# Kernel optimization log

Hardware: AMD Instinct MI355X
Metric: run time of the kernel (lower is better)

The kernel has to match this reference:

```python
import jax, jax.numpy as jnp
import numpy as np

B, F, D = 1024, 160000, 16


def setup_inputs() -> dict:
    key = jax.random.key(0)
    k1, k2, k3 = jax.random.split(key, 3)
    x = jax.random.randint(k1, (B, F), 0, 2, dtype=jnp.int32)  # multi-hot transaction
    emb_w = jax.random.normal(k2, (F, D), dtype=jnp.float32) * 0.05  # FM factor table
    bias_w = jax.random.normal(k3, (F, 1), dtype=jnp.float32) * 0.05  # per-field linear bias
    g_bias = jnp.zeros((), dtype=jnp.float32)  # global bias
    return {"x": x, "emb_w": emb_w, "bias_w": bias_w, "g_bias": g_bias}


def reference(x, emb_w, bias_w, g_bias):
    # mask[b,f] = 1 where field f is active (row > 0 in original tf code)
    mask = (x > 0).astype(emb_w.dtype)  # [B, F]
    # sum of active embeddings per row: equals gather+sum in the original
    ev = mask @ emb_w  # [B, D]
    # sum of squared norms of active embeddings per row
    rowsq = jnp.sum(emb_w * emb_w, axis=1)  # [F]
    sum_sq = mask @ rowsq  # [B]
    # 0.5 * (sum_{i,j} e_i . e_j - sum_i ||e_i||^2) == FM pairwise interaction
    second = 0.5 * (jnp.sum(ev * ev, axis=-1) - sum_sq)  # [B]
    # linear term: global bias + sum of active field biases
    linear = g_bias + mask @ bias_w  # [B, 1]
    return linear + second[:, None]  # [B, 1]
```

## Files before the change

kernel.cpp:

```cpp
#include <hip/hip_runtime.h>
#include <hip/hip_bf16.h>

#define B_ROWS 1024
#define F_FLD  160000
#define D_DIM  16
#define TCOLS  256
#define NCHUNK (F_FLD / TCOLS)
#define NKB    (F_FLD / 32)
#define NSTAT  (D_DIM + 1)
#define ACC_N  (B_ROWS * NSTAT)
#define RED_SLAB 25

typedef __attribute__((ext_vector_type(8))) short bf16x8;
typedef __attribute__((ext_vector_type(4))) float f32x4;

static __device__ inline unsigned short f2bf(float x) {
    __hip_bfloat16 h = __float2bfloat16(x);
    union { __hip_bfloat16 h; unsigned short s; } u; u.h = h; return u.s;
}

static __device__ inline bf16x8 expand8(unsigned b) {
    union { unsigned u[4]; bf16x8 v; } r;
    r.u[0] = ((b        & 1u) * 0x3F80u) | (((b >> 1) & 1u) * 0x3F800000u);
    r.u[1] = (((b >> 2) & 1u) * 0x3F80u) | (((b >> 3) & 1u) * 0x3F800000u);
    r.u[2] = (((b >> 4) & 1u) * 0x3F80u) | (((b >> 5) & 1u) * 0x3F800000u);
    r.u[3] = (((b >> 6) & 1u) * 0x3F80u) | (((b >> 7) & 1u) * 0x3F800000u);
    return r.v;
}

__global__ __launch_bounds__(256) void fm_prep(const float* __restrict__ emb,
                                               const float* __restrict__ bias,
                                               float* __restrict__ c,
                                               float* __restrict__ acc) {
    int i = blockIdx.x * 256 + threadIdx.x;
    if (i < F_FLD) {
        const float4* e = (const float4*)(emb + (size_t)i * D_DIM);
        float4 e0 = e[0], e1 = e[1], e2 = e[2], e3 = e[3];
        float s = e0.x*e0.x + e0.y*e0.y + e0.z*e0.z + e0.w*e0.w
                + e1.x*e1.x + e1.y*e1.y + e1.z*e1.z + e1.w*e1.w
                + e2.x*e2.x + e2.y*e2.y + e2.z*e2.z + e2.w*e2.w
                + e3.x*e3.x + e3.y*e3.y + e3.z*e3.z + e3.w*e3.w;
        c[i] = bias[i] - 0.5f * s;
    }
    if (i < ACC_N) acc[i] = 0.0f;
}

__global__ __launch_bounds__(256) void fm_pack(const float* __restrict__ emb,
                                               const float* __restrict__ c,
                                               unsigned short* __restrict__ embB,
                                               unsigned short* __restrict__ cB2c) {
    const int tid = threadIdx.x;
    const int kb = blockIdx.x * 4 + (tid >> 6);
    const int l = tid & 63, q = l >> 4, n = l & 15;
    union { unsigned short s[8]; uint4 u; } v;
#pragma unroll
    for (int j = 0; j < 8; ++j) {
        int f = kb * 32 + 4 * j + q;
        v.s[j] = f2bf(emb[(size_t)f * D_DIM + n]);
    }
    *(uint4*)(embB + ((size_t)kb * 64 + l) * 8) = v.u;
    if (n == 0) {
        union { unsigned short s[8]; uint4 u; } w;
#pragma unroll
        for (int j = 0; j < 8; ++j) w.s[j] = f2bf(c[kb * 32 + 4 * j + q]);
        *(uint4*)(cB2c + ((size_t)kb * 4 + q) * 8) = w.u;
    }
}

__global__ __launch_bounds__(256) void fm_main(const int* __restrict__ x,
                                               const unsigned short* __restrict__ embB,
                                               const unsigned short* __restrict__ cB2c,
                                               float* __restrict__ partial,
                                               float* __restrict__ acc,
                                               int use_partial) {
    __shared__ unsigned long long msk[256][4];
    const int tid = threadIdx.x;
    const int w = tid >> 6, l = tid & 63;
    const int q = l >> 4, n = l & 15;
    const int rowbase = blockIdx.y * 256;
    const int c0 = blockIdx.x * TCOLS;
    const int kb0 = blockIdx.x * 8;

    {
        const int4* xp = (const int4*)(x + (size_t)(rowbase + w * 64) * F_FLD + c0) + l;
        const size_t rstr = F_FLD / 4;
        for (int i = 0; i < 64; i += 8) {
            int4 v[8];
#pragma unroll
            for (int k = 0; k < 8; ++k) v[k] = xp[(size_t)(i + k) * rstr];
#pragma unroll
            for (int k = 0; k < 8; ++k) {
                unsigned long long m0 = __ballot(v[k].x > 0);
                unsigned long long m1 = __ballot(v[k].y > 0);
                unsigned long long m2 = __ballot(v[k].z > 0);
                unsigned long long m3 = __ballot(v[k].w > 0);
                if (l == 0) {
                    int r = w * 64 + i + k;
                    msk[r][0] = m0; msk[r][1] = m1; msk[r][2] = m2; msk[r][3] = m3;
                }
            }
        }
    }

    unsigned long long wq[4];
#pragma unroll
    for (int mt = 0; mt < 4; ++mt) wq[mt] = msk[w * 64 + mt * 16 + n][q];

    f32x4 aev[4], ac[4];
#pragma unroll
    for (int mt = 0; mt < 4; ++mt) {
        aev[mt] = (f32x4){0.f, 0.f, 0.f, 0.f};
        ac[mt]  = (f32x4){0.f, 0.f, 0.f, 0.f};
    }

    const uint4* eB = (const uint4*)embB;
    const uint4* cB = (const uint4*)cB2c;
#pragma unroll
    for (int s = 0; s < 8; ++s) {
        union { uint4 u; bf16x8 v; } Bf, Cf;
        Bf.u = eB[(size_t)(kb0 + s) * 64 + l];
        Cf.u = cB[(size_t)(kb0 + s) * 4 + q];
#pragma unroll
        for (int mt = 0; mt < 4; ++mt) {
            unsigned b = (unsigned)(wq[mt] >> (8 * s)) & 0xFFu;
            bf16x8 A = expand8(b);
            aev[mt] = __builtin_amdgcn_mfma_f32_16x16x32_bf16(A, Bf.v, aev[mt], 0, 0, 0);
            ac[mt]  = __builtin_amdgcn_mfma_f32_16x16x32_bf16(A, Cf.v, ac[mt], 0, 0, 0);
        }
    }

    const int ch = blockIdx.x;
#pragma unroll
    for (int mt = 0; mt < 4; ++mt) {
        int rowg = rowbase + w * 64 + mt * 16 + q * 4;
        if (use_partial) {
#pragma unroll
            for (int r = 0; r < 4; ++r) {
                float* p = partial + ((size_t)ch * B_ROWS + rowg + r) * NSTAT;
                p[n] = aev[mt][r];
                if (n == 0) p[16] = ac[mt][r];
            }
        } else {
#pragma unroll
            for (int r = 0; r < 4; ++r) {
                atomicAdd(acc + (size_t)(rowg + r) * NSTAT + n, aev[mt][r]);
                if (n == 0) atomicAdd(acc + (size_t)(rowg + r) * NSTAT + 16, ac[mt][r]);
            }
        }
    }
}

__global__ __launch_bounds__(256) void fm_reduce(const float* __restrict__ partial,
                                                 float* __restrict__ acc) {
    int t = blockIdx.x * 256 + threadIdx.x;
    if (t >= ACC_N) return;
    const float* p = partial + (size_t)blockIdx.y * RED_SLAB * ACC_N + t;
    float s = 0.0f;
#pragma unroll 5
    for (int k = 0; k < RED_SLAB; ++k) s += p[(size_t)k * ACC_N];
    atomicAdd(acc + t, s);
}

__global__ __launch_bounds__(256) void fm_final(const float* __restrict__ acc,
                                                const float* __restrict__ g_bias,
                                                float* __restrict__ out) {
    int row = blockIdx.x * 256 + threadIdx.x;
    if (row >= B_ROWS) return;
    const float* a = acc + (size_t)row * NSTAT;
    float s = 0.0f;
#pragma unroll
    for (int d = 0; d < D_DIM; ++d) s += a[d] * a[d];
    out[row] = g_bias[0] + a[16] + 0.5f * s;
}

extern "C" void kernel_launch(void* const* d_in, const int* in_sizes, int n_in,
                              void* d_out, int out_size, void* d_ws, size_t ws_size,
                              hipStream_t stream) {
    const int*   x      = (const int*)d_in[0];
    const float* emb_w  = (const float*)d_in[1];
    const float* bias_w = (const float*)d_in[2];
    const float* g_bias = (const float*)d_in[3];
    float*       out    = (float*)d_out;

    size_t off_c    = 0;
    size_t off_acc  = off_c   + (size_t)F_FLD * 4;
    size_t off_embB = off_acc + (size_t)ACC_N * 4;
    size_t off_cB   = off_embB + (size_t)NKB * 64 * 8 * 2;
    size_t off_par  = off_cB  + (size_t)NKB * 4 * 8 * 2;
    size_t total    = off_par + (size_t)NCHUNK * B_ROWS * NSTAT * 4;

    float*          c       = (float*)((char*)d_ws + off_c);
    float*          acc     = (float*)((char*)d_ws + off_acc);
    unsigned short* embB    = (unsigned short*)((char*)d_ws + off_embB);
    unsigned short* cB2c    = (unsigned short*)((char*)d_ws + off_cB);
    float*          partial = (float*)((char*)d_ws + off_par);
    int use_partial = (ws_size >= total) ? 1 : 0;

    fm_prep<<<dim3((F_FLD + 255) / 256), dim3(256), 0, stream>>>(emb_w, bias_w, c, acc);
    fm_pack<<<dim3(NKB / 4), dim3(256), 0, stream>>>(emb_w, c, embB, cB2c);
    fm_main<<<dim3(NCHUNK, B_ROWS / 256), dim3(256), 0, stream>>>(
        x, embB, cB2c, partial, acc, use_partial);
    if (use_partial)
        fm_reduce<<<dim3((ACC_N + 255) / 256, NCHUNK / RED_SLAB), dim3(256), 0, stream>>>(
            partial, acc);
    fm_final<<<dim3((B_ROWS + 255) / 256), dim3(256), 0, stream>>>(acc, g_bias, out);
}
```

Before: 858.1 us.

## Retile FM main kernel to wide column chunks with in-block reduction, fuse prep

The main kernel now gives each block 16 rows by 6400 columns with 8 waves splitting the K dimension. Partials are reduced in shared memory and then atomically added, which removes the large partial buffer and the separate reduce kernel. The prep and pack kernels are merged: squared norms are computed with lane shuffles while packing, and acc is zeroed in the same pass. The trade-off is that each row's embedding tile is now reloaded across 64 row blocks instead of 4, which raises reuse traffic on the bf16 table through L2, and more atomics land per output element.

New measurement: 849.5 us (median of 2 runs). No clear change (-1.0%).

```diff
diff --git a/kernel.cpp b/kernel.cpp
--- a/kernel.cpp
+++ b/kernel.cpp
@@ -4,12 +4,15 @@
 #define B_ROWS 1024
 #define F_FLD  160000
 #define D_DIM  16
-#define TCOLS  256
-#define NCHUNK (F_FLD / TCOLS)
 #define NKB    (F_FLD / 32)
 #define NSTAT  (D_DIM + 1)
 #define ACC_N  (B_ROWS * NSTAT)
-#define RED_SLAB 25
+#define CCOLS  6400
+#define NGRP   (CCOLS / 256)
+#define KBC    (CCOLS / 32)
+#define NCHUNK (F_FLD / CCOLS)
+#define ROWS_B 16
+#define WAVES  8
 
 typedef __attribute__((ext_vector_type(8))) short bf16x8;
 typedef __attribute__((ext_vector_type(4))) float f32x4;
@@ -28,137 +31,111 @@
     return r.v;
 }
 
-__global__ __launch_bounds__(256) void fm_prep(const float* __restrict__ emb,
+__global__ __launch_bounds__(256) void fm_pack(const float* __restrict__ emb,
                                                const float* __restrict__ bias,
-                                               float* __restrict__ c,
+                                               unsigned short* __restrict__ embB,
+                                               unsigned short* __restrict__ cB2c,
                                                float* __restrict__ acc) {
-    int i = blockIdx.x * 256 + threadIdx.x;
-    if (i < F_FLD) {
-        const float4* e = (const float4*)(emb + (size_t)i * D_DIM);
-        float4 e0 = e[0], e1 = e[1], e2 = e[2], e3 = e[3];
-        float s = e0.x*e0.x + e0.y*e0.y + e0.z*e0.z + e0.w*e0.w
-                + e1.x*e1.x + e1.y*e1.y + e1.z*e1.z + e1.w*e1.w
-                + e2.x*e2.x + e2.y*e2.y + e2.z*e2.z + e2.w*e2.w
-                + e3.x*e3.x + e3.y*e3.y + e3.z*e3.z + e3.w*e3.w;
-        c[i] = bias[i] - 0.5f * s;
-    }
-    if (i < ACC_N) acc[i] = 0.0f;
-}
-
-__global__ __launch_bounds__(256) void fm_pack(const float* __restrict__ emb,
-                                               const float* __restrict__ c,
-                                               unsigned short* __restrict__ embB,
-                                               unsigned short* __restrict__ cB2c) {
     const int tid = threadIdx.x;
     const int kb = blockIdx.x * 4 + (tid >> 6);
     const int l = tid & 63, q = l >> 4, n = l & 15;
+
+    float e[8];
     union { unsigned short s[8]; uint4 u; } v;
 #pragma unroll
     for (int j = 0; j < 8; ++j) {
         int f = kb * 32 + 4 * j + q;
-        v.s[j] = f2bf(emb[(size_t)f * D_DIM + n]);
+        e[j] = emb[(size_t)f * D_DIM + n];
+        v.s[j] = f2bf(e[j]);
     }
     *(uint4*)(embB + ((size_t)kb * 64 + l) * 8) = v.u;
-    if (n == 0) {
-        union { unsigned short s[8]; uint4 u; } w;
+
+    union { unsigned short s[8]; uint4 u; } w;
 #pragma unroll
-        for (int j = 0; j < 8; ++j) w.s[j] = f2bf(c[kb * 32 + 4 * j + q]);
-        *(uint4*)(cB2c + ((size_t)kb * 4 + q) * 8) = w.u;
+    for (int j = 0; j < 8; ++j) {
+        float s = e[j] * e[j];
+        s += __shfl_xor(s, 1);
+        s += __shfl_xor(s, 2);
+        s += __shfl_xor(s, 4);
+        s += __shfl_xor(s, 8);
+        int f = kb * 32 + 4 * j + q;
+        w.s[j] = f2bf((n == 0 ? bias[f] : 0.0f) - 0.5f * s);
     }
+    if (n == 0) *(uint4*)(cB2c + ((size_t)kb * 4 + q) * 8) = w.u;
+
+    int gid = blockIdx.x * 256 + tid;
+    if (gid < ACC_N) acc[gid] = 0.0f;
 }
 
-__global__ __launch_bounds__(256) void fm_main(const int* __restrict__ x,
-                                               const unsigned short* __restrict__ embB,
-                                               const unsigned short* __restrict__ cB2c,
-                                               float* __restrict__ partial,
-                                               float* __restrict__ acc,
-                                               int use_partial) {
-    __shared__ unsigned long long msk[256][4];
+__global__ __launch_bounds__(512, 6) void fm_main(const int* __restrict__ x,
+                                                  const unsigned short* __restrict__ embB,
+                                                  const unsigned short* __restrict__ cB2c,
+                                                  float* __restrict__ acc) {
+    __shared__ unsigned long long msk[NGRP][ROWS_B][4];
+    __shared__ float red[WAVES][ROWS_B][NSTAT];
+
     const int tid = threadIdx.x;
     const int w = tid >> 6, l = tid & 63;
     const int q = l >> 4, n = l & 15;
-    const int rowbase = blockIdx.y * 256;
-    const int c0 = blockIdx.x * TCOLS;
-    const int kb0 = blockIdx.x * 8;
+    const int rowbase = blockIdx.y * ROWS_B;
+    const int c0 = blockIdx.x * CCOLS;
 
-    {
-        const int4* xp = (const int4*)(x + (size_t)(rowbase + w * 64) * F_FLD + c0) + l;
-        const size_t rstr = F_FLD / 4;
-        for (int i = 0; i < 64; i += 8) {
-            int4 v[8];
 #pragma unroll
-            for (int k = 0; k < 8; ++k) v[k] = xp[(size_t)(i + k) * rstr];
+    for (int rr = 0; rr < 2; ++rr) {
+        const int rloc = 2 * w + rr;
+        const int4* xp = (const int4*)(x + (size_t)(rowbase + rloc) * F_FLD + c0) + l;
+        for (int g0 = 0; g0 < NGRP; g0 += 5) {
+            int4 v[5];
 #pragma unroll
-            for (int k = 0; k < 8; ++k) {
+            for (int k = 0; k < 5; ++k) v[k] = xp[(size_t)(g0 + k) * 64];
+#pragma unroll
+            for (int k = 0; k < 5; ++k) {
                 unsigned long long m0 = __ballot(v[k].x > 0);
                 unsigned long long m1 = __ballot(v[k].y > 0);
                 unsigned long long m2 = __ballot(v[k].z > 0);
                 unsigned long long m3 = __ballot(v[k].w > 0);
                 if (l == 0) {
-                    int r = w * 64 + i + k;
-                    msk[r][0] = m0; msk[r][1] = m1; msk[r][2] = m2; msk[r][3] = m3;
+                    msk[g0 + k][rloc][0] = m0; msk[g0 + k][rloc][1] = m1;
+                    msk[g0 + k][rloc][2] = m2; msk[g0 + k][rloc][3] = m3;
                 }
             }
         }
     }
+    __syncthreads();
 
-    unsigned long long wq[4];
-#pragma unroll
-    for (int mt = 0; mt < 4; ++mt) wq[mt] = msk[w * 64 + mt * 16 + n][q];
+    f32x4 aev = {0.f, 0.f, 0.f, 0.f}, ac = {0.f, 0.f, 0.f, 0.f};
+    const uint4* eB = (const uint4*)embB;
+    const uint4* cB = (const uint4*)cB2c;
+    const int kbg0 = blockIdx.x * KBC;
 
-    f32x4 aev[4], ac[4];
-#pragma unroll
-    for (int mt = 0; mt < 4; ++mt) {
-        aev[mt] = (f32x4){0.f, 0.f, 0.f, 0.f};
-        ac[mt]  = (f32x4){0.f, 0.f, 0.f, 0.f};
+#pragma unroll 2
+    for (int t = 0; t < KBC / WAVES; ++t) {
+        const int kb = w * (KBC / WAVES) + t;
+        const int g = kb >> 3, byt = kb & 7;
+        unsigned long long mv = msk[g][n][q];
+        unsigned b = (unsigned)(mv >> (8 * byt)) & 0xFFu;
+        bf16x8 A = expand8(b);
+        union { uint4 u; bf16x8 v; } Bf, Cf;
+        Bf.u = eB[(size_t)(kbg0 + kb) * 64 + l];
+        Cf.u = cB[(size_t)(kbg0 + kb) * 4 + q];
+        aev = __builtin_amdgcn_mfma_f32_16x16x32_bf16(A, Bf.v, aev, 0, 0, 0);
+        ac  = __builtin_amdgcn_mfma_f32_16x16x32_bf16(A, Cf.v, ac,  0, 0, 0);
     }
 
-    const uint4* eB = (const uint4*)embB;
-    const uint4* cB = (const uint4*)cB2c;
 #pragma unroll
-    for (int s = 0; s < 8; ++s) {
-        union { uint4 u; bf16x8 v; } Bf, Cf;
-        Bf.u = eB[(size_t)(kb0 + s) * 64 + l];
-        Cf.u = cB[(size_t)(kb0 + s) * 4 + q];
+    for (int r = 0; r < 4; ++r) {
+        red[w][q * 4 + r][n] = aev[r];
+        if (n == 0) red[w][q * 4 + r][16] = ac[r];
+    }
+    __syncthreads();
+
+    if (tid < ROWS_B * NSTAT) {
+        int row = tid / NSTAT, col = tid % NSTAT;
+        float s = 0.0f;
 #pragma unroll
-        for (int mt = 0; mt < 4; ++mt) {
-            unsigned b = (unsigned)(wq[mt] >> (8 * s)) & 0xFFu;
-            bf16x8 A = expand8(b);
-            aev[mt] = __builtin_amdgcn_mfma_f32_16x16x32_bf16(A, Bf.v, aev[mt], 0, 0, 0);
-            ac[mt]  = __builtin_amdgcn_mfma_f32_16x16x32_bf16(A, Cf.v, ac[mt], 0, 0, 0);
-        }
+        for (int ww = 0; ww < WAVES; ++ww) s += red[ww][row][col];
+        atomicAdd(acc + (size_t)(rowbase + row) * NSTAT + col, s);
     }
-
-    const int ch = blockIdx.x;
-#pragma unroll
-    for (int mt = 0; mt < 4; ++mt) {
-        int rowg = rowbase + w * 64 + mt * 16 + q * 4;
-        if (use_partial) {
-#pragma unroll
-            for (int r = 0; r < 4; ++r) {
-                float* p = partial + ((size_t)ch * B_ROWS + rowg + r) * NSTAT;
-                p[n] = aev[mt][r];
-                if (n == 0) p[16] = ac[mt][r];
-            }
-        } else {
-#pragma unroll
-            for (int r = 0; r < 4; ++r) {
-                atomicAdd(acc + (size_t)(rowg + r) * NSTAT + n, aev[mt][r]);
-                if (n == 0) atomicAdd(acc + (size_t)(rowg + r) * NSTAT + 16, ac[mt][r]);
-            }
-        }
-    }
-}
-
-__global__ __launch_bounds__(256) void fm_reduce(const float* __restrict__ partial,
-                                                 float* __restrict__ acc) {
-    int t = blockIdx.x * 256 + threadIdx.x;
-    if (t >= ACC_N) return;
-    const float* p = partial + (size_t)blockIdx.y * RED_SLAB * ACC_N + t;
-    float s = 0.0f;
-#pragma unroll 5
-    for (int k = 0; k < RED_SLAB; ++k) s += p[(size_t)k * ACC_N];
-    atomicAdd(acc + t, s);
 }
 
 __global__ __launch_bounds__(256) void fm_final(const float* __restrict__ acc,
@@ -182,26 +159,12 @@
     const float* g_bias = (const float*)d_in[3];
     float*       out    = (float*)d_out;
 
-    size_t off_c    = 0;
-    size_t off_acc  = off_c   + (size_t)F_FLD * 4;
-    size_t off_embB = off_acc + (size_t)ACC_N * 4;
-    size_t off_cB   = off_embB + (size_t)NKB * 64 * 8 * 2;
-    size_t off_par  = off_cB  + (size_t)NKB * 4 * 8 * 2;
-    size_t total    = off_par + (size_t)NCHUNK * B_ROWS * NSTAT * 4;
+    unsigned short* embB = (unsigned short*)d_ws;
+    unsigned short* cB2c = (unsigned short*)((char*)d_ws + (size_t)NKB * 64 * 8 * 2);
+    float*          acc  = (float*)((char*)d_ws + (size_t)NKB * 64 * 8 * 2
+                                                + (size_t)NKB * 4 * 8 * 2);
 
-    float*          c       = (float*)((char*)d_ws + off_c);
-    float*          acc     = (float*)((char*)d_ws + off_acc);
-    unsigned short* embB    = (unsigned short*)((char*)d_ws + off_embB);
-    unsigned short* cB2c    = (unsigned short*)((char*)d_ws + off_cB);
-    float*          partial = (float*)((char*)d_ws + off_par);
-    int use_partial = (ws_size >= total) ? 1 : 0;
-
-    fm_prep<<<dim3((F_FLD + 255) / 256), dim3(256), 0, stream>>>(emb_w, bias_w, c, acc);
-    fm_pack<<<dim3(NKB / 4), dim3(256), 0, stream>>>(emb_w, c, embB, cB2c);
-    fm_main<<<dim3(NCHUNK, B_ROWS / 256), dim3(256), 0, stream>>>(
-        x, embB, cB2c, partial, acc, use_partial);
-    if (use_partial)
-        fm_reduce<<<dim3((ACC_N + 255) / 256, NCHUNK / RED_SLAB), dim3(256), 0, stream>>>(
-            partial, acc);
+    fm_pack<<<dim3(NKB / 4), dim3(256), 0, stream>>>(emb_w, bias_w, embB, cB2c, acc);
+    fm_main<<<dim3(NCHUNK, B_ROWS / ROWS_B), dim3(512), 0, stream>>>(x, embB, cB2c, acc);
     fm_final<<<dim3((B_ROWS + 255) / 256), dim3(256), 0, stream>>>(acc, g_bias, out);
 }
```
